# Optimization experiments

Hardware: AMD Instinct MI355X
Metric: run time of the kernel (lower is better)

The kernel has to match this reference:

```python
import jax, jax.numpy as jnp
import numpy as np

B, N, E = 1024, 156, 1564
C_IN, C_HID, C_OUT = 301, 128, 128
BN_EPS = 1e-5


def setup_inputs() -> dict:
    key = jax.random.key(0)
    ks = jax.random.split(key, 12)
    x = jax.random.normal(ks[0], (B, N, C_IN), dtype=jnp.float32)
    edge_index = jax.random.randint(ks[1], (2, E), 0, N, dtype=jnp.int64)
    # GCNConv linear weights (PyG lin has no bias; conv bias added after aggregation)
    W0 = jax.random.normal(ks[2], (C_IN, C_HID), dtype=jnp.float32) / np.sqrt(C_IN)
    b0 = jnp.zeros((C_HID,), dtype=jnp.float32)
    W1 = jax.random.normal(ks[3], (C_HID, C_HID), dtype=jnp.float32) / np.sqrt(C_HID)
    b1 = jnp.zeros((C_HID,), dtype=jnp.float32)
    W2 = jax.random.normal(ks[4], (C_HID, C_OUT), dtype=jnp.float32) / np.sqrt(C_HID)
    b2 = jnp.zeros((C_OUT,), dtype=jnp.float32)
    # BatchNorm affine params (eval mode: running_mean=0, running_var=1)
    bn_w0 = jax.random.uniform(ks[5], (C_HID,), dtype=jnp.float32, minval=0.5, maxval=1.5)
    bn_b0 = jax.random.normal(ks[6], (C_HID,), dtype=jnp.float32) * 0.1
    bn_w1 = jax.random.uniform(ks[7], (C_HID,), dtype=jnp.float32, minval=0.5, maxval=1.5)
    bn_b1 = jax.random.normal(ks[8], (C_HID,), dtype=jnp.float32) * 0.1
    return {"x": x, "edge_index": edge_index,
            "W0": W0, "b0": b0, "bn_w0": bn_w0, "bn_b0": bn_b0,
            "W1": W1, "b1": b1, "bn_w1": bn_w1, "bn_b1": bn_b1,
            "W2": W2, "b2": b2}


def _gcn_norm(edge_index, num_nodes):
    # add self-loops, compute symmetric normalization deg^-1/2[src]*deg^-1/2[dst]
    loops = jnp.tile(jnp.arange(num_nodes, dtype=edge_index.dtype)[None, :], (2, 1))
    ei = jnp.concatenate([edge_index, loops], axis=1)  # [2, E+N]
    row, col = ei[0], ei[1]
    deg = jnp.zeros((num_nodes,), dtype=jnp.float32).at[col].add(1.0)
    dinv = jnp.where(deg > 0, deg ** -0.5, 0.0)
    return row, col, dinv[row] * dinv[col]


def _gcn_conv(h, row, col, norm, W, b):
    # h: [B, N, Cin] -> [B, N, Cout]
    h = jnp.einsum('bnc,co->bno', h, W)
    msg = h[:, row, :] * norm[None, :, None]          # [B, E+N, Cout]
    out = jnp.zeros_like(h).at[:, col, :].add(msg)    # scatter-add to dst nodes
    return out + b


def _bn_eval(h, w, b):
    # eval-mode BatchNorm1d with running_mean=0, running_var=1
    return h * (w / jnp.sqrt(1.0 + BN_EPS)) + b


def reference(x, edge_index, W0, b0, bn_w0, bn_b0, W1, b1, bn_w1, bn_b1, W2, b2):
    n = x.shape[1]
    row, col, norm = _gcn_norm(edge_index, n)
    h = jax.nn.relu(_bn_eval(_gcn_conv(x, row, col, norm, W0, b0), bn_w0, bn_b0))
    h = jax.nn.relu(_bn_eval(_gcn_conv(h, row, col, norm, W1, b1), bn_w1, bn_b1))
    return _gcn_conv(h, row, col, norm, W2, b2)
```

## Files before the change

kernel.cpp:

```cpp
#include <hip/hip_runtime.h>

#define NN    156
#define NP    160
#define CN    128
#define K0    301
#define KP0   320
#define BATCH 1024

#define W0_OFF 0
#define W1_OFF (128 * KP0)
#define W2_OFF (128 * KP0 + 128 * 128)

typedef __attribute__((ext_vector_type(8))) short bf16x8;
typedef __attribute__((ext_vector_type(4))) float f32x4;

__device__ __align__(16) ushort g_WtH[128 * (KP0 + 128 + 128)];
__device__ __align__(16) ushort g_WtL[128 * (KP0 + 128 + 128)];
__device__ __align__(16) ushort g_AdjH[NP * NP];
__device__ __align__(16) ushort g_AdjL[NP * NP];

__device__ __forceinline__ ushort bf16_rne(float f) {
    return __builtin_bit_cast(ushort, (__bf16)f);
}
__device__ __forceinline__ float bf16_f(ushort h) {
    return __builtin_bit_cast(float, (uint32_t)h << 16);
}
__device__ __forceinline__ ushort bf16_lo(float f, ushort h) {
    return (ushort)(__builtin_bit_cast(uint32_t, f - bf16_f(h)) >> 16);
}

__device__ __forceinline__ void barrier_lgkm() {
    asm volatile("s_waitcnt lgkmcnt(0)\n\ts_barrier" ::: "memory");
}

__global__ __launch_bounds__(256) void prep_wt(const int* __restrict__ ei, int E,
        const float* __restrict__ W0, const float* __restrict__ W1,
        const float* __restrict__ W2, const float* __restrict__ bw0,
        const float* __restrict__ bw1) {
    __shared__ float adjf[NP * NP];
    __shared__ int   cnt[NP];
    __shared__ float dinv_s[NP];
    const int t = threadIdx.x;
    if (blockIdx.x == 0) {
        for (int i = t; i < NP * NP; i += 256) adjf[i] = 0.f;
        for (int n = t; n < NP; n += 256) cnt[n] = (n < NN) ? 1 : 0;
        __syncthreads();
        for (int e = t; e < E; e += 256) atomicAdd(&cnt[ei[E + e]], 1);
        __syncthreads();
        for (int n = t; n < NP; n += 256)
            dinv_s[n] = (cnt[n] > 0) ? rsqrtf((float)cnt[n]) : 0.f;
        __syncthreads();
        for (int e = t; e < E; e += 256) {
            const int r = ei[e], c = ei[E + e];
            atomicAdd(&adjf[c * NP + r], dinv_s[r] * dinv_s[c]);
        }
        for (int n = t; n < NN; n += 256)
            atomicAdd(&adjf[n * NP + n], dinv_s[n] * dinv_s[n]);
        __syncthreads();
        for (int i = t; i < NP * NP; i += 256) {
            const float v = adjf[i];
            const ushort h = bf16_rne(v);
            g_AdjH[i] = h;
            g_AdjL[i] = bf16_lo(v, h);
        }
    } else {
        const int id = (blockIdx.x - 1) * 256 + t;
        const float* W; int K, KP, woff, local;
        if (id < 128 * KP0)              { W = W0; K = K0;  KP = KP0; woff = W0_OFF; local = id; }
        else if (id < 128 * (KP0 + 128)) { W = W1; K = 128; KP = 128; woff = W1_OFF; local = id - 128 * KP0; }
        else                             { W = W2; K = 128; KP = 128; woff = W2_OFF; local = id - 128 * (KP0 + 128); }
        const int n = local & 127, k = local >> 7;
        const float inv = rsqrtf(1.f + 1e-5f);
        float s = 1.f;
        if (woff == W0_OFF) s = bw0[n] * inv;
        else if (woff == W1_OFF) s = bw1[n] * inv;
        const float f = (k < K) ? W[(size_t)k * CN + n] * s : 0.f;
        const ushort h = bf16_rne(f);
        g_WtH[woff + n * KP + k] = h;
        g_WtL[woff + n * KP + k] = bf16_lo(f, h);
    }
}

__global__ __launch_bounds__(256, 2) void fused_all(
        const float* __restrict__ x,
        const float* __restrict__ cb0, const float* __restrict__ bw0, const float* __restrict__ bb0,
        const float* __restrict__ cb1, const float* __restrict__ bw1, const float* __restrict__ bb1,
        const float* __restrict__ cb2, float* __restrict__ out) {
    __shared__ __align__(16) uint8_t smem[81920];
    uint8_t* const pH = smem;
    uint8_t* const pL = smem + 40960;

    const int t = threadIdx.x;
    const int lane = t & 63, wave = t >> 6;
    const int quad = lane >> 4, l15 = lane & 15;
    const int wr = (wave >> 1) * 80;
    const int wc = (wave & 1) * 64;
    const int ac = (wave & 1) * 64;
    const int ad = (wave >> 1) * 80;
    const size_t arow0 = (size_t)blockIdx.x * NN;

    f32x4 acc[5][4];
    f32x4 og[4][5];

    const int kp  = (t & 15) * 2;
    const int r0s = t >> 4;
    float sv0[10], sv1[10];

    auto stage_load = [&](int kt) {
        const int kk = kt * 32 + kp;
#pragma unroll
        for (int s = 0; s < 10; s++) {
            const int r  = r0s + s * 16;
            const int rc = (r < NN) ? r : (NN - 1);
            const size_t abase = (arow0 + rc) * (size_t)K0;
            sv0[s] = (kk < K0)     ? x[abase + kk]     : 0.f;
            sv1[s] = (kk + 1 < K0) ? x[abase + kk + 1] : 0.f;
        }
    };
    auto stage_write = [&](int buf) {
        const int segoff = buf * 10240 + (((kp >> 3) * NP) << 4) + (kp & 7) * 2;
#pragma unroll
        for (int s = 0; s < 10; s++) {
            const int off = segoff + ((r0s + s * 16) << 4);
            const ushort h0 = bf16_rne(sv0[s]), h1 = bf16_rne(sv1[s]);
            *(ushort2*)(pH + off) = make_ushort2(h0, h1);
            *(ushort2*)(pL + off) = make_ushort2(bf16_lo(sv0[s], h0), bf16_lo(sv1[s], h1));
        }
    };

    bf16x8 wbH[2][4], wbL[2][4];
    auto loadW = [&](int woff, int KP, int kt, int sl) {
#pragma unroll
        for (int j = 0; j < 4; j++) {
            const int wi = woff + (wc + j * 16 + l15) * KP + kt * 32 + quad * 8;
            wbH[sl][j] = *(const bf16x8*)&g_WtH[wi];
            wbL[sl][j] = *(const bf16x8*)&g_WtL[wi];
        }
    };

    bf16x8 gjH[4], gjL[4];
    auto adj_pf = [&](int step) {
        const int k2 = step / 5, nj = step % 5;
        const int ai = (ad + nj * 16 + l15) * NP + k2 * 32 + quad * 8;
        gjH[step & 3] = *(const bf16x8*)&g_AdjH[ai];
        gjL[step & 3] = *(const bf16x8*)&g_AdjL[ai];
    };

    auto gemm_l0_tile = [&](int buf, int sl) {
#pragma unroll
        for (int i = 0; i < 5; i++) {
            const int off = buf * 10240 + ((quad * NP + wr + i * 16 + l15) << 4);
            const bf16x8 aH = *(const bf16x8*)(pH + off);
            const bf16x8 aL = *(const bf16x8*)(pL + off);
#pragma unroll
            for (int j = 0; j < 4; j++) {
                acc[i][j] = __builtin_amdgcn_mfma_f32_16x16x32_bf16(aH, wbH[sl][j], acc[i][j], 0, 0, 0);
                acc[i][j] = __builtin_amdgcn_mfma_f32_16x16x32_bf16(aH, wbL[sl][j], acc[i][j], 0, 0, 0);
                acc[i][j] = __builtin_amdgcn_mfma_f32_16x16x32_bf16(aL, wbH[sl][j], acc[i][j], 0, 0, 0);
            }
        }
    };

    auto gemm_h = [&](int woff) {
#pragma unroll
        for (int i = 0; i < 5; i++)
#pragma unroll
            for (int j = 0; j < 4; j++) acc[i][j] = (f32x4){0.f, 0.f, 0.f, 0.f};
#pragma unroll
        for (int kt = 0; kt < 4; kt++) {
            if (kt < 3) loadW(woff, CN, kt + 1, (kt + 1) & 1);
#pragma unroll
            for (int i = 0; i < 5; i++) {
                const int off = ((kt * 4 + quad) * NP + wr + i * 16 + l15) << 4;
                const bf16x8 aH = *(const bf16x8*)(pH + off);
                const bf16x8 aL = *(const bf16x8*)(pL + off);
#pragma unroll
                for (int j = 0; j < 4; j++) {
                    acc[i][j] = __builtin_amdgcn_mfma_f32_16x16x32_bf16(aH, wbH[kt & 1][j], acc[i][j], 0, 0, 0);
                    acc[i][j] = __builtin_amdgcn_mfma_f32_16x16x32_bf16(aH, wbL[kt & 1][j], acc[i][j], 0, 0, 0);
                    acc[i][j] = __builtin_amdgcn_mfma_f32_16x16x32_bf16(aL, wbH[kt & 1][j], acc[i][j], 0, 0, 0);
                }
            }
        }
    };

    auto write_tT = [&]() {
#pragma unroll
        for (int i = 0; i < 5; i++)
#pragma unroll
            for (int j = 0; j < 4; j++) {
                const int ch = wc + j * 16 + l15;
                const int s0 = wr + i * 16 + quad * 4;
                const int off = (((s0 >> 3) * CN + ch) << 4) + (s0 & 7) * 2;
                ushort4 hs, ls;
#pragma unroll
                for (int rg = 0; rg < 4; rg++) {
                    const float v = acc[i][j][rg];
                    const ushort h = bf16_rne(v);
                    (&hs.x)[rg] = h;
                    (&ls.x)[rg] = bf16_lo(v, h);
                }
                *(ushort4*)(pH + off) = hs;
                *(ushort4*)(pL + off) = ls;
            }
    };

    auto do_agg = [&]() {
#pragma unroll
        for (int mi = 0; mi < 4; mi++)
#pragma unroll
            for (int nj = 0; nj < 5; nj++) og[mi][nj] = (f32x4){0.f, 0.f, 0.f, 0.f};
#pragma unroll
        for (int k2 = 0; k2 < 5; k2++) {
            bf16x8 taH[4], taL[4];
#pragma unroll
            for (int mi = 0; mi < 4; mi++) {
                const int off = ((k2 * 4 + quad) * CN + ac + mi * 16 + l15) << 4;
                taH[mi] = *(const bf16x8*)(pH + off);
                taL[mi] = *(const bf16x8*)(pL + off);
            }
#pragma unroll
            for (int nj = 0; nj < 5; nj++) {
                const int step = k2 * 5 + nj, slot = step & 3;
#pragma unroll
                for (int mi = 0; mi < 4; mi++) {
                    og[mi][nj] = __builtin_amdgcn_mfma_f32_16x16x32_bf16(taH[mi], gjH[slot], og[mi][nj], 0, 0, 0);
                    og[mi][nj] = __builtin_amdgcn_mfma_f32_16x16x32_bf16(taH[mi], gjL[slot], og[mi][nj], 0, 0, 0);
                    og[mi][nj] = __builtin_amdgcn_mfma_f32_16x16x32_bf16(taL[mi], gjH[slot], og[mi][nj], 0, 0, 0);
                }
                if (step + 4 < 25) adj_pf(step + 4);
            }
        }
    };

    auto write_h = [&](const float* cb, const float* bw, const float* bb) {
        const float inv = rsqrtf(1.f + 1e-5f);
#pragma unroll
        for (int mi = 0; mi < 4; mi++) {
            const int c0 = ac + mi * 16 + quad * 4;
            const float4 cbv = *(const float4*)&cb[c0];
            const float4 bwv = *(const float4*)&bw[c0];
            const float4 bbv = *(const float4*)&bb[c0];
            float cbf[4];
#pragma unroll
            for (int rg = 0; rg < 4; rg++)
                cbf[rg] = fmaf((&cbv.x)[rg], (&bwv.x)[rg] * inv, (&bbv.x)[rg]);
#pragma unroll
            for (int nj = 0; nj < 5; nj++) {
                const int node = ad + nj * 16 + l15;
                const int off = (((c0 >> 3) * NP + node) << 4) + (c0 & 7) * 2;
                ushort4 hs, ls;
#pragma unroll
                for (int rg = 0; rg < 4; rg++) {
                    const float v = fmaxf(og[mi][nj][rg] + cbf[rg], 0.f);
                    const ushort h = bf16_rne(v);
                    (&hs.x)[rg] = h;
                    (&ls.x)[rg] = bf16_lo(v, h);
                }
                *(ushort4*)(pH + off) = hs;
                *(ushort4*)(pL + off) = ls;
            }
        }
    };

    auto write_out = [&](const float* cb) {
#pragma unroll
        for (int mi = 0; mi < 4; mi++) {
            const int c0 = ac + mi * 16 + quad * 4;
            const float4 cbv = *(const float4*)&cb[c0];
#pragma unroll
            for (int nj = 0; nj < 5; nj++) {
                const int node = ad + nj * 16 + l15;
                if (node < NN) {
                    float4 o;
#pragma unroll
                    for (int rg = 0; rg < 4; rg++)
                        (&o.x)[rg] = og[mi][nj][rg] + (&cbv.x)[rg];
                    *(float4*)&out[(arow0 + node) * CN + c0] = o;
                }
            }
        }
    };

#pragma unroll
    for (int i = 0; i < 5; i++)
#pragma unroll
        for (int j = 0; j < 4; j++) acc[i][j] = (f32x4){0.f, 0.f, 0.f, 0.f};
    stage_load(0);
    stage_write(0);
    loadW(W0_OFF, KP0, 0, 0);
    barrier_lgkm();
#pragma unroll
    for (int kt = 0; kt < 10; kt++) {
        if (kt < 9) stage_load(kt + 1);
        if (kt < 9) loadW(W0_OFF, KP0, kt + 1, (kt + 1) & 1);
        gemm_l0_tile(kt & 1, kt & 1);
        if (kt < 9) stage_write((kt + 1) & 1);
        barrier_lgkm();
    }
    write_tT();
    adj_pf(0); adj_pf(1); adj_pf(2); adj_pf(3);
    barrier_lgkm();
    do_agg();
    barrier_lgkm();
    write_h(cb0, bw0, bb0);
    loadW(W1_OFF, CN, 0, 0);
    barrier_lgkm();
    gemm_h(W1_OFF);
    barrier_lgkm();
    write_tT();
    adj_pf(0); adj_pf(1); adj_pf(2); adj_pf(3);
    barrier_lgkm();
    do_agg();
    barrier_lgkm();
    write_h(cb1, bw1, bb1);
    loadW(W2_OFF, CN, 0, 0);
    barrier_lgkm();
    gemm_h(W2_OFF);
    barrier_lgkm();
    write_tT();
    adj_pf(0); adj_pf(1); adj_pf(2); adj_pf(3);
    barrier_lgkm();
    do_agg();
    write_out(cb2);
}

extern "C" void kernel_launch(void* const* d_in, const int* in_sizes, int n_in,
                              void* d_out, int out_size, void* d_ws, size_t ws_size,
                              hipStream_t stream) {
    const float* x    = (const float*)d_in[0];
    const int*   ei   = (const int*)  d_in[1];
    const float* W0   = (const float*)d_in[2];
    const float* b0   = (const float*)d_in[3];
    const float* bnw0 = (const float*)d_in[4];
    const float* bnb0 = (const float*)d_in[5];
    const float* W1   = (const float*)d_in[6];
    const float* b1   = (const float*)d_in[7];
    const float* bnw1 = (const float*)d_in[8];
    const float* bnb1 = (const float*)d_in[9];
    const float* W2   = (const float*)d_in[10];
    const float* b2   = (const float*)d_in[11];
    float* out = (float*)d_out;

    const int E = in_sizes[1] / 2;

    prep_wt<<<289, 256, 0, stream>>>(ei, E, W0, W1, W2, bnw0, bnw1);
    fused_all<<<BATCH, 256, 0, stream>>>(x, b0, bnw0, bnb0,
                                         b1, bnw1, bnb1, b2, out);
}
```

Baseline: 448.5 us.

## Process two graphs per 512-thread block, sharing weight and adjacency fragments

Each block now handles two batch graphs with eight waves. Each wave covers 32 output channels instead of 64, and every weight and adjacency fragment it loads is reused for both graphs, which halves per-graph global and L2 traffic for those operands. The layer-0 staging moves to 64-wide K tiles with an XOR-swizzled row-major LDS layout, so there are half as many pipeline barriers and fewer LDS bank conflicts. The cost is 160KB of LDS per block, which allows only one block per CU, and barriers now span eight waves, which can reduce latency hiding between blocks.

```diff
diff --git a/kernel.cpp b/kernel.cpp
--- a/kernel.cpp
+++ b/kernel.cpp
@@ -6,6 +6,7 @@
 #define K0    301
 #define KP0   320
 #define BATCH 1024
+#define NG    2
 
 #define W0_OFF 0
 #define W1_OFF (128 * KP0)
@@ -81,61 +82,184 @@
     }
 }
 
-__global__ __launch_bounds__(256, 2) void fused_all(
+__global__ __launch_bounds__(512, 2) void fused_all(
         const float* __restrict__ x,
         const float* __restrict__ cb0, const float* __restrict__ bw0, const float* __restrict__ bb0,
         const float* __restrict__ cb1, const float* __restrict__ bw1, const float* __restrict__ bb1,
         const float* __restrict__ cb2, float* __restrict__ out) {
-    __shared__ __align__(16) uint8_t smem[81920];
-    uint8_t* const pH = smem;
-    uint8_t* const pL = smem + 40960;
+    __shared__ __align__(16) uint8_t smem[163840];
 
     const int t = threadIdx.x;
     const int lane = t & 63, wave = t >> 6;
     const int quad = lane >> 4, l15 = lane & 15;
-    const int wr = (wave >> 1) * 80;
-    const int wc = (wave & 1) * 64;
-    const int ac = (wave & 1) * 64;
-    const int ad = (wave >> 1) * 80;
-    const size_t arow0 = (size_t)blockIdx.x * NN;
-
-    f32x4 acc[5][4];
-    f32x4 og[4][5];
-
-    const int kp  = (t & 15) * 2;
+    const int wr = (wave >> 2) * 80;
+    const int wc = (wave & 3) * 32;
+    const int ac = (wave & 3) * 32;
+    const int ad = (wave >> 2) * 80;
+
+    uint8_t* const pH[NG] = { smem,         smem + 81920 };
+    uint8_t* const pL[NG] = { smem + 40960, smem + 122880 };
+
+    size_t arow0[NG];
+    arow0[0] = (size_t)(blockIdx.x * 2) * NN;
+    arow0[1] = arow0[0] + NN;
+
+    f32x4 acc[NG][5][2];
+    f32x4 og[NG][2][5];
+
     const int r0s = t >> 4;
-    float sv0[10], sv1[10];
+    const int c4  = t & 15;
+    float sv[NG][5][4];
 
     auto stage_load = [&](int kt) {
-        const int kk = kt * 32 + kp;
-#pragma unroll
-        for (int s = 0; s < 10; s++) {
-            const int r  = r0s + s * 16;
-            const int rc = (r < NN) ? r : (NN - 1);
-            const size_t abase = (arow0 + rc) * (size_t)K0;
-            sv0[s] = (kk < K0)     ? x[abase + kk]     : 0.f;
-            sv1[s] = (kk + 1 < K0) ? x[abase + kk + 1] : 0.f;
-        }
+        const int kk = kt * 64 + c4 * 4;
+#pragma unroll
+        for (int g = 0; g < NG; g++)
+#pragma unroll
+            for (int s = 0; s < 5; s++) {
+                const int r  = r0s + s * 32;
+                const int rc = (r < NN) ? r : (NN - 1);
+                const float* xp = x + (arow0[g] + rc) * (size_t)K0;
+#pragma unroll
+                for (int e = 0; e < 4; e++)
+                    sv[g][s][e] = (kk + e < K0) ? xp[kk + e] : 0.f;
+            }
     };
     auto stage_write = [&](int buf) {
-        const int segoff = buf * 10240 + (((kp >> 3) * NP) << 4) + (kp & 7) * 2;
-#pragma unroll
-        for (int s = 0; s < 10; s++) {
-            const int off = segoff + ((r0s + s * 16) << 4);
-            const ushort h0 = bf16_rne(sv0[s]), h1 = bf16_rne(sv1[s]);
-            *(ushort2*)(pH + off) = make_ushort2(h0, h1);
-            *(ushort2*)(pL + off) = make_ushort2(bf16_lo(sv0[s], h0), bf16_lo(sv1[s], h1));
-        }
-    };
-
-    bf16x8 wbH[2][4], wbL[2][4];
-    auto loadW = [&](int woff, int KP, int kt, int sl) {
-#pragma unroll
-        for (int j = 0; j < 4; j++) {
-            const int wi = woff + (wc + j * 16 + l15) * KP + kt * 32 + quad * 8;
+#pragma unroll
+        for (int g = 0; g < NG; g++)
+#pragma unroll
+            for (int s = 0; s < 5; s++) {
+                const int r = r0s + s * 32;
+                const int koct = (c4 >> 1) ^ (r & 7);
+                const int off = buf * 20480 + (r * 8 + koct) * 16 + (c4 & 1) * 8;
+                ushort4 hs, ls;
+#pragma unroll
+                for (int e = 0; e < 4; e++) {
+                    const float v = sv[g][s][e];
+                    const ushort h = bf16_rne(v);
+                    (&hs.x)[e] = h;
+                    (&ls.x)[e] = bf16_lo(v, h);
+                }
+                *(ushort4*)(pH[g] + off) = hs;
+                *(ushort4*)(pL[g] + off) = ls;
+            }
+    };
+
+    bf16x8 wH[2][2], wL[2][2];
+    auto loadW0 = [&](int kt) {
+#pragma unroll
+        for (int ks = 0; ks < 2; ks++)
+#pragma unroll
+            for (int j = 0; j < 2; j++) {
+                const int wi = W0_OFF + (wc + j * 16 + l15) * KP0 + kt * 64 + ks * 32 + quad * 8;
+                wH[ks][j] = *(const bf16x8*)&g_WtH[wi];
+                wL[ks][j] = *(const bf16x8*)&g_WtL[wi];
+            }
+    };
+    auto gemm_l0 = [&](int buf) {
+#pragma unroll
+        for (int ks = 0; ks < 2; ks++)
+#pragma unroll
+            for (int g = 0; g < NG; g++)
+#pragma unroll
+            for (int i = 0; i < 5; i++) {
+                const int row = wr + i * 16 + l15;
+                const int off = buf * 20480 + (row * 8 + ((ks * 4 + quad) ^ (row & 7))) * 16;
+                const bf16x8 aH = *(const bf16x8*)(pH[g] + off);
+                const bf16x8 aL = *(const bf16x8*)(pL[g] + off);
+#pragma unroll
+                for (int j = 0; j < 2; j++) {
+                    acc[g][i][j] = __builtin_amdgcn_mfma_f32_16x16x32_bf16(aH, wH[ks][j], acc[g][i][j], 0, 0, 0);
+                    acc[g][i][j] = __builtin_amdgcn_mfma_f32_16x16x32_bf16(aH, wL[ks][j], acc[g][i][j], 0, 0, 0);
+                    acc[g][i][j] = __builtin_amdgcn_mfma_f32_16x16x32_bf16(aL, wH[ks][j], acc[g][i][j], 0, 0, 0);
+                }
+            }
+    };
+
+    bf16x8 wbH[2][2], wbL[2][2];
+    auto loadWh = [&](int woff, int kt, int sl) {
+#pragma unroll
+        for (int j = 0; j < 2; j++) {
+            const int wi = woff + (wc + j * 16 + l15) * CN + kt * 32 + quad * 8;
             wbH[sl][j] = *(const bf16x8*)&g_WtH[wi];
             wbL[sl][j] = *(const bf16x8*)&g_WtL[wi];
         }
+    };
+    auto gemm_h = [&]() {
+#pragma unroll
+        for (int g = 0; g < NG; g++)
+#pragma unroll
+            for (int i = 0; i < 5; i++)
+#pragma unroll
+                for (int j = 0; j < 2; j++) acc[g][i][j] = (f32x4){0.f, 0.f, 0.f, 0.f};
+#pragma unroll
+        for (int kt = 0; kt < 4; kt++) {
+#pragma unroll
+            for (int g = 0; g < NG; g++)
+#pragma unroll
+            for (int i = 0; i < 5; i++) {
+                const int off = ((kt * 4 + quad) * NP + wr + i * 16 + l15) << 4;
+                const bf16x8 aH = *(const bf16x8*)(pH[g] + off);
+                const bf16x8 aL = *(const bf16x8*)(pL[g] + off);
+#pragma unroll
+                for (int j = 0; j < 2; j++) {
+                    acc[g][i][j] = __builtin_amdgcn_mfma_f32_16x16x32_bf16(aH, wbH[kt & 1][j], acc[g][i][j], 0, 0, 0);
+                    acc[g][i][j] = __builtin_amdgcn_mfma_f32_16x16x32_bf16(aH, wbL[kt & 1][j], acc[g][i][j], 0, 0, 0);
+                    acc[g][i][j] = __builtin_amdgcn_mfma_f32_16x16x32_bf16(aL, wbH[kt & 1][j], acc[g][i][j], 0, 0, 0);
+                }
+            }
+        }
+    };
+    auto gemm_h_full = [&](int woff) {
+#pragma unroll
+        for (int g = 0; g < NG; g++)
+#pragma unroll
+            for (int i = 0; i < 5; i++)
+#pragma unroll
+                for (int j = 0; j < 2; j++) acc[g][i][j] = (f32x4){0.f, 0.f, 0.f, 0.f};
+#pragma unroll
+        for (int kt = 0; kt < 4; kt++) {
+            if (kt < 3) loadWh(woff, kt + 1, (kt + 1) & 1);
+#pragma unroll
+            for (int g = 0; g < NG; g++)
+#pragma unroll
+            for (int i = 0; i < 5; i++) {
+                const int off = ((kt * 4 + quad) * NP + wr + i * 16 + l15) << 4;
+                const bf16x8 aH = *(const bf16x8*)(pH[g] + off);
+                const bf16x8 aL = *(const bf16x8*)(pL[g] + off);
+#pragma unroll
+                for (int j = 0; j < 2; j++) {
+                    acc[g][i][j] = __builtin_amdgcn_mfma_f32_16x16x32_bf16(aH, wbH[kt & 1][j], acc[g][i][j], 0, 0, 0);
+                    acc[g][i][j] = __builtin_amdgcn_mfma_f32_16x16x32_bf16(aH, wbL[kt & 1][j], acc[g][i][j], 0, 0, 0);
+                    acc[g][i][j] = __builtin_amdgcn_mfma_f32_16x16x32_bf16(aL, wbH[kt & 1][j], acc[g][i][j], 0, 0, 0);
+                }
+            }
+        }
+    };
+    (void)gemm_h;
+
+    auto write_tT = [&]() {
+#pragma unroll
+        for (int g = 0; g < NG; g++)
+#pragma unroll
+        for (int i = 0; i < 5; i++)
+#pragma unroll
+            for (int j = 0; j < 2; j++) {
+                const int ch = wc + j * 16 + l15;
+                const int s0 = wr + i * 16 + quad * 4;
+                const int off = (((s0 >> 3) * CN + ch) << 4) + (s0 & 7) * 2;
+                ushort4 hs, ls;
+#pragma unroll
+                for (int rg = 0; rg < 4; rg++) {
+                    const float v = acc[g][i][j][rg];
+                    const ushort h = bf16_rne(v);
+                    (&hs.x)[rg] = h;
+                    (&ls.x)[rg] = bf16_lo(v, h);
+                }
+                *(ushort4*)(pH[g] + off) = hs;
+                *(ushort4*)(pL[g] + off) = ls;
+            }
     };
 
     bf16x8 gjH[4], gjL[4];
@@ -146,87 +270,34 @@
         gjL[step & 3] = *(const bf16x8*)&g_AdjL[ai];
     };
 
-    auto gemm_l0_tile = [&](int buf, int sl) {
-#pragma unroll
-        for (int i = 0; i < 5; i++) {
-            const int off = buf * 10240 + ((quad * NP + wr + i * 16 + l15) << 4);
-            const bf16x8 aH = *(const bf16x8*)(pH + off);
-            const bf16x8 aL = *(const bf16x8*)(pL + off);
-#pragma unroll
-            for (int j = 0; j < 4; j++) {
-                acc[i][j] = __builtin_amdgcn_mfma_f32_16x16x32_bf16(aH, wbH[sl][j], acc[i][j], 0, 0, 0);
-                acc[i][j] = __builtin_amdgcn_mfma_f32_16x16x32_bf16(aH, wbL[sl][j], acc[i][j], 0, 0, 0);
-                acc[i][j] = __builtin_amdgcn_mfma_f32_16x16x32_bf16(aL, wbH[sl][j], acc[i][j], 0, 0, 0);
-            }
-        }
-    };
-
-    auto gemm_h = [&](int woff) {
-#pragma unroll
-        for (int i = 0; i < 5; i++)
-#pragma unroll
-            for (int j = 0; j < 4; j++) acc[i][j] = (f32x4){0.f, 0.f, 0.f, 0.f};
-#pragma unroll
-        for (int kt = 0; kt < 4; kt++) {
-            if (kt < 3) loadW(woff, CN, kt + 1, (kt + 1) & 1);
-#pragma unroll
-            for (int i = 0; i < 5; i++) {
-                const int off = ((kt * 4 + quad) * NP + wr + i * 16 + l15) << 4;
-                const bf16x8 aH = *(const bf16x8*)(pH + off);
-                const bf16x8 aL = *(const bf16x8*)(pL + off);
-#pragma unroll
-                for (int j = 0; j < 4; j++) {
-                    acc[i][j] = __builtin_amdgcn_mfma_f32_16x16x32_bf16(aH, wbH[kt & 1][j], acc[i][j], 0, 0, 0);
-                    acc[i][j] = __builtin_amdgcn_mfma_f32_16x16x32_bf16(aH, wbL[kt & 1][j], acc[i][j], 0, 0, 0);
-                    acc[i][j] = __builtin_amdgcn_mfma_f32_16x16x32_bf16(aL, wbH[kt & 1][j], acc[i][j], 0, 0, 0);
-                }
-            }
-        }
-    };
-
-    auto write_tT = [&]() {
-#pragma unroll
-        for (int i = 0; i < 5; i++)
-#pragma unroll
-            for (int j = 0; j < 4; j++) {
-                const int ch = wc + j * 16 + l15;
-                const int s0 = wr + i * 16 + quad * 4;
-                const int off = (((s0 >> 3) * CN + ch) << 4) + (s0 & 7) * 2;
-                ushort4 hs, ls;
-#pragma unroll
-                for (int rg = 0; rg < 4; rg++) {
-                    const float v = acc[i][j][rg];
-                    const ushort h = bf16_rne(v);
-                    (&hs.x)[rg] = h;
-                    (&ls.x)[rg] = bf16_lo(v, h);
-                }
-                *(ushort4*)(pH + off) = hs;
-                *(ushort4*)(pL + off) = ls;
-            }
-    };
-
     auto do_agg = [&]() {
 #pragma unroll
-        for (int mi = 0; mi < 4; mi++)
-#pragma unroll
-            for (int nj = 0; nj < 5; nj++) og[mi][nj] = (f32x4){0.f, 0.f, 0.f, 0.f};
+        for (int g = 0; g < NG; g++)
+#pragma unroll
+            for (int mi = 0; mi < 2; mi++)
+#pragma unroll
+                for (int nj = 0; nj < 5; nj++) og[g][mi][nj] = (f32x4){0.f, 0.f, 0.f, 0.f};
 #pragma unroll
         for (int k2 = 0; k2 < 5; k2++) {
-            bf16x8 taH[4], taL[4];
-#pragma unroll
-            for (int mi = 0; mi < 4; mi++) {
-                const int off = ((k2 * 4 + quad) * CN + ac + mi * 16 + l15) << 4;
-                taH[mi] = *(const bf16x8*)(pH + off);
-                taL[mi] = *(const bf16x8*)(pL + off);
-            }
+            bf16x8 taH[NG][2], taL[NG][2];
+#pragma unroll
+            for (int g = 0; g < NG; g++)
+#pragma unroll
+                for (int mi = 0; mi < 2; mi++) {
+                    const int off = ((k2 * 4 + quad) * CN + ac + mi * 16 + l15) << 4;
+                    taH[g][mi] = *(const bf16x8*)(pH[g] + off);
+                    taL[g][mi] = *(const bf16x8*)(pL[g] + off);
+                }
 #pragma unroll
             for (int nj = 0; nj < 5; nj++) {
                 const int step = k2 * 5 + nj, slot = step & 3;
 #pragma unroll
-                for (int mi = 0; mi < 4; mi++) {
-                    og[mi][nj] = __builtin_amdgcn_mfma_f32_16x16x32_bf16(taH[mi], gjH[slot], og[mi][nj], 0, 0, 0);
-                    og[mi][nj] = __builtin_amdgcn_mfma_f32_16x16x32_bf16(taH[mi], gjL[slot], og[mi][nj], 0, 0, 0);
-                    og[mi][nj] = __builtin_amdgcn_mfma_f32_16x16x32_bf16(taL[mi], gjH[slot], og[mi][nj], 0, 0, 0);
+                for (int g = 0; g < NG; g++)
+#pragma unroll
+                for (int mi = 0; mi < 2; mi++) {
+                    og[g][mi][nj] = __builtin_amdgcn_mfma_f32_16x16x32_bf16(taH[g][mi], gjH[slot], og[g][mi][nj], 0, 0, 0);
+                    og[g][mi][nj] = __builtin_amdgcn_mfma_f32_16x16x32_bf16(taH[g][mi], gjL[slot], og[g][mi][nj], 0, 0, 0);
+                    og[g][mi][nj] = __builtin_amdgcn_mfma_f32_16x16x32_bf16(taL[g][mi], gjH[slot], og[g][mi][nj], 0, 0, 0);
                 }
                 if (step + 4 < 25) adj_pf(step + 4);
             }
@@ -236,7 +307,7 @@
     auto write_h = [&](const float* cb, const float* bw, const float* bb) {
         const float inv = rsqrtf(1.f + 1e-5f);
 #pragma unroll
-        for (int mi = 0; mi < 4; mi++) {
+        for (int mi = 0; mi < 2; mi++) {
             const int c0 = ac + mi * 16 + quad * 4;
             const float4 cbv = *(const float4*)&cb[c0];
             const float4 bwv = *(const float4*)&bw[c0];
@@ -246,28 +317,32 @@
             for (int rg = 0; rg < 4; rg++)
                 cbf[rg] = fmaf((&cbv.x)[rg], (&bwv.x)[rg] * inv, (&bbv.x)[rg]);
 #pragma unroll
+            for (int g = 0; g < NG; g++)
+#pragma unroll
             for (int nj = 0; nj < 5; nj++) {
                 const int node = ad + nj * 16 + l15;
                 const int off = (((c0 >> 3) * NP + node) << 4) + (c0 & 7) * 2;
                 ushort4 hs, ls;
 #pragma unroll
                 for (int rg = 0; rg < 4; rg++) {
-                    const float v = fmaxf(og[mi][nj][rg] + cbf[rg], 0.f);
+                    const float v = fmaxf(og[g][mi][nj][rg] + cbf[rg], 0.f);
                     const ushort h = bf16_rne(v);
                     (&hs.x)[rg] = h;
                     (&ls.x)[rg] = bf16_lo(v, h);
                 }
-                *(ushort4*)(pH + off) = hs;
-                *(ushort4*)(pL + off) = ls;
+                *(ushort4*)(pH[g] + off) = hs;
+                *(ushort4*)(pL[g] + off) = ls;
             }
         }
     };
 
     auto write_out = [&](const float* cb) {
 #pragma unroll
-        for (int mi = 0; mi < 4; mi++) {
+        for (int mi = 0; mi < 2; mi++) {
             const int c0 = ac + mi * 16 + quad * 4;
             const float4 cbv = *(const float4*)&cb[c0];
+#pragma unroll
+            for (int g = 0; g < NG; g++)
 #pragma unroll
             for (int nj = 0; nj < 5; nj++) {
                 const int node = ad + nj * 16 + l15;
@@ -275,27 +350,28 @@
                     float4 o;
 #pragma unroll
                     for (int rg = 0; rg < 4; rg++)
-                        (&o.x)[rg] = og[mi][nj][rg] + (&cbv.x)[rg];
-                    *(float4*)&out[(arow0 + node) * CN + c0] = o;
-                }
-            }
-        }
-    };
-
-#pragma unroll
-    for (int i = 0; i < 5; i++)
-#pragma unroll
-        for (int j = 0; j < 4; j++) acc[i][j] = (f32x4){0.f, 0.f, 0.f, 0.f};
+                        (&o.x)[rg] = og[g][mi][nj][rg] + (&cbv.x)[rg];
+                    *(float4*)&out[(arow0[g] + node) * CN + c0] = o;
+                }
+            }
+        }
+    };
+
+#pragma unroll
+    for (int g = 0; g < NG; g++)
+#pragma unroll
+        for (int i = 0; i < 5; i++)
+#pragma unroll
+            for (int j = 0; j < 2; j++) acc[g][i][j] = (f32x4){0.f, 0.f, 0.f, 0.f};
     stage_load(0);
     stage_write(0);
-    loadW(W0_OFF, KP0, 0, 0);
-    barrier_lgkm();
-#pragma unroll
-    for (int kt = 0; kt < 10; kt++) {
-        if (kt < 9) stage_load(kt + 1);
-        if (kt < 9) loadW(W0_OFF, KP0, kt + 1, (kt + 1) & 1);
-        gemm_l0_tile(kt & 1, kt & 1);
-        if (kt < 9) stage_write((kt + 1) & 1);
+    loadW0(0);
+    barrier_lgkm();
+#pragma unroll
+    for (int kt = 0; kt < 5; kt++) {
+        if (kt < 4) stage_load(kt + 1);
+        gemm_l0(kt & 1);
+        if (kt < 4) { loadW0(kt + 1); stage_write((kt + 1) & 1); }
         barrier_lgkm();
     }
     write_tT();
@@ -304,9 +380,9 @@
     do_agg();
     barrier_lgkm();
     write_h(cb0, bw0, bb0);
-    loadW(W1_OFF, CN, 0, 0);
-    barrier_lgkm();
-    gemm_h(W1_OFF);
+    loadWh(W1_OFF, 0, 0);
+    barrier_lgkm();
+    gemm_h_full(W1_OFF);
     barrier_lgkm();
     write_tT();
     adj_pf(0); adj_pf(1); adj_pf(2); adj_pf(3);
@@ -314,9 +390,9 @@
     do_agg();
     barrier_lgkm();
     write_h(cb1, bw1, bb1);
-    loadW(W2_OFF, CN, 0, 0);
-    barrier_lgkm();
-    gemm_h(W2_OFF);
+    loadWh(W2_OFF, 0, 0);
+    barrier_lgkm();
+    gemm_h_full(W2_OFF);
     barrier_lgkm();
     write_tT();
     adj_pf(0); adj_pf(1); adj_pf(2); adj_pf(3);
@@ -345,6 +421,6 @@
     const int E = in_sizes[1] / 2;
 
     prep_wt<<<289, 256, 0, stream>>>(ei, E, W0, W1, W2, bnw0, bnw1);
-    fused_all<<<BATCH, 256, 0, stream>>>(x, b0, bnw0, bnb0,
-                                         b1, bnw1, bnb1, b2, out);
-}
+    fused_all<<<BATCH / NG, 512, 0, stream>>>(x, b0, bnw0, bnb0,
+                                              b1, bnw1, bnb1, b2, out);
+}
```

Measured after the change: 452.8 us. No clear change (+1.0%).
